# Kernel tuning notes

Hardware: AMD Instinct MI355X
Metric: run time of the kernel (lower is better)

## Reference

```python
import jax, jax.numpy as jnp
import numpy as np

B = 8192
D, T = 40, 100      # input_dim = [D, T]
P, Q = 120, 100     # output_dim = [P, Q]


def setup_inputs() -> dict:
    key = jax.random.key(0)
    ks = jax.random.split(key, 6)
    s = 0.05  # keep pre-softmax logits in a sane range
    return {
        "X": jax.random.normal(ks[0], (B, D, T), dtype=jnp.float32),
        "W1": jax.random.normal(ks[1], (P, D), dtype=jnp.float32) * s,
        "W": jax.random.normal(ks[2], (T, T), dtype=jnp.float32) * s,
        "alpha": jax.random.uniform(ks[3], (1,), dtype=jnp.float32),
        "W2": jax.random.normal(ks[4], (T, Q), dtype=jnp.float32) * s,
        "bias": jax.random.normal(ks[5], (P, Q), dtype=jnp.float32) * s,
    }


def reference(X, W1, W, alpha, W2, bias):
    # X: [B, D, T]
    X1 = jnp.einsum("pd,bdt->bpt", W1, X)          # per-sample W1 @ X[i]
    E = jnp.einsum("bpt,ts->bps", X1, W)            # per-sample X1[i] @ W
    # Faithful to torch: nn.Softmax() with dim=None on a 3D tensor -> dim 0 (batch)
    A = jax.nn.softmax(E, axis=0)                   # [B, P, T]
    tem = alpha * (X1 * A) + (1.0 - alpha) * X1     # alpha-gated attention blend
    Y = jnp.einsum("bpt,tq->bpq", tem, W2) + bias   # [B, P, Q]
    # output_dim[1] == Q == 100 != 1, so the squeeze branch is not taken
    return Y
```

## Files before the change

### kernel.cpp

```cpp
#include <hip/hip_runtime.h>


typedef __attribute__((ext_vector_type(8))) short short8;
typedef __attribute__((ext_vector_type(4))) float floatx4;

constexpr int Bb = 8192;

constexpr int ST1 = 136;
constexpr int ST2 = 72;

constexpr int XB_B   = 48  * ST1 * 2;
constexpr int XWT_B  = 112 * ST2 * 2;
constexpr int WT_B   = 112 * ST1 * 2;
constexpr int W2T_B  = 112 * ST1 * 2;
constexpr int XT_B   = 112 * ST2 * 2;
constexpr int X1A_B  = 128 * ST1 * 2;

constexpr int WS_S_BYTES = 48000;
constexpr int WTG_OFF  = 48000;
constexpr int W1G_OFF  = WTG_OFF + WT_B;
constexpr int W2TG_OFF = W1G_OFF + 128 * ST2 * 2;

constexpr int P1_XB  = 0;
constexpr int P1_XWT = XB_B;
constexpr int P1_WT  = P1_XWT + XWT_B;
constexpr int P1_LDS = P1_WT + WT_B;

constexpr int P2_WB  = X1A_B;
constexpr int P2_LDS = P2_WB + WT_B;

constexpr int NB1 = 16;
constexpr int NB2 = 32;

constexpr int WCHUNKS = WT_B / 16;

__device__ __forceinline__ unsigned short f2bf(float f) {
  union { float f; unsigned u; } v; v.f = f;
  return (unsigned short)((v.u + 0x7FFFu + ((v.u >> 16) & 1u)) >> 16);
}

__device__ __forceinline__ void copy16(void* dst, const void* src, int nbytes,
                                       int tid, int nthr) {
  int4* d = (int4*)dst; const int4* s = (const int4*)src;
  const int n = nbytes >> 4;
  for (int i = tid; i < n; i += nthr) d[i] = s[i];
}

__global__ void tabl_prep(const float* __restrict__ W1, const float* __restrict__ W,
                          const float* __restrict__ W2, char* ws) {
  int i = blockIdx.x * 256 + threadIdx.x;
  if (i < 112 * ST1) {
    int s = i / ST1, t = i % ST1;
    ((unsigned short*)(ws + WTG_OFF))[i] = (s < 100 && t < 100) ? f2bf(W[t * 100 + s]) : 0;
  } else if (i < 112 * ST1 + 128 * ST2) {
    int j = i - 112 * ST1;
    int p = j / ST2, d = j % ST2;
    ((unsigned short*)(ws + W1G_OFF))[j] = (p < 120 && d < 40) ? f2bf(W1[p * 40 + d]) : 0;
  } else if (i < 112 * ST1 + 128 * ST2 + 112 * ST1) {
    int j = i - 112 * ST1 - 128 * ST2;
    int q = j / ST1, t = j % ST1;
    ((unsigned short*)(ws + W2TG_OFF))[j] = (q < 100 && t < 100) ? f2bf(W2[t * 100 + q]) : 0;
  }
}

__global__ __launch_bounds__(256, 2)
void tabl_ph1(const float* __restrict__ X, const char* __restrict__ ws,
              float* __restrict__ S) {
  __shared__ __align__(16) char smem[P1_LDS];
  short* Xb  = (short*)(smem + P1_XB);
  short* XWt = (short*)(smem + P1_XWT);
  short* Wt  = (short*)(smem + P1_WT);

  const int tid = threadIdx.x;
  const int wid = tid >> 6, lane = tid & 63;
  const int quad = lane >> 4, r = lane & 15;
  const floatx4 zed = {0.f, 0.f, 0.f, 0.f};

  short8 w1f[2][2];
#pragma unroll
  for (int h = 0; h < 2; ++h)
#pragma unroll
    for (int ks = 0; ks < 2; ++ks)
      w1f[h][ks] = *(const short8*)(ws + W1G_OFF +
          2 * (((2 * wid + h) * 16 + r) * ST2 + ks * 32 + quad * 8));

  copy16(Wt, ws + WTG_OFF, WT_B, tid, 256);
  for (int i = tid; i < 8 * ST1; i += 256) {
    int dd = 40 + i / ST1, tt = i % ST1; Xb[dd * ST1 + tt] = 0;
  }
  for (int i = tid; i < 40 * 28; i += 256) {
    int dd = i / 28, tt = 100 + i % 28; Xb[dd * ST1 + tt] = 0;
  }
  for (int i = tid; i < 112 * 16; i += 256) {
    int rr = i / 16, cc = 48 + i % 16; XWt[rr * ST2 + cc] = 0;
  }

  const int b0 = blockIdx.x * NB1;
  {
    const float4* x4 = (const float4*)(X + (size_t)b0 * 4000);
#pragma unroll
    for (int k = 0; k < 4; ++k) {
      int idx = tid + k * 256;
      if (idx < 1000) {
        float4 v = x4[idx];
        short4 pk; pk.x = (short)f2bf(v.x); pk.y = (short)f2bf(v.y);
        pk.z = (short)f2bf(v.z); pk.w = (short)f2bf(v.w);
        int e0 = idx * 4, d = e0 / 100, t = e0 - d * 100;
        *(short4*)&Xb[d * ST1 + t] = pk;
      }
    }
  }

  floatx4 sacc[2][7];
#pragma unroll
  for (int h = 0; h < 2; ++h)
#pragma unroll
    for (int n = 0; n < 7; ++n) sacc[h][n] = zed;

  for (int nb = 0; nb < NB1; ++nb) {
    __syncthreads();

    float4 xr[4];
    const bool pf = (nb + 1 < NB1);
    if (pf) {
      const float4* x4n = (const float4*)(X + (size_t)(b0 + nb + 1) * 4000);
#pragma unroll
      for (int k = 0; k < 4; ++k) {
        int idx = tid + k * 256;
        if (idx < 1000) xr[k] = x4n[idx];
      }
    }

    floatx4 xw[2][3];
#pragma unroll
    for (int ns = 0; ns < 2; ++ns)
#pragma unroll
      for (int m = 0; m < 3; ++m) xw[ns][m] = zed;
#pragma unroll
    for (int ks = 0; ks < 4; ++ks) {
      short8 a0 = *(const short8*)&Xb[(0 * 16 + r) * ST1 + ks * 32 + quad * 8];
      short8 a1 = *(const short8*)&Xb[(1 * 16 + r) * ST1 + ks * 32 + quad * 8];
      short8 a2 = *(const short8*)&Xb[(2 * 16 + r) * ST1 + ks * 32 + quad * 8];
#pragma unroll
      for (int ns = 0; ns < 2; ++ns) {
        int ni = wid + ns * 4;
        if (ni < 7) {
          short8 bf = *(const short8*)&Wt[(ni * 16 + r) * ST1 + ks * 32 + quad * 8];
          xw[ns][0] = __builtin_amdgcn_mfma_f32_16x16x32_bf16(a0, bf, xw[ns][0], 0, 0, 0);
          xw[ns][1] = __builtin_amdgcn_mfma_f32_16x16x32_bf16(a1, bf, xw[ns][1], 0, 0, 0);
          xw[ns][2] = __builtin_amdgcn_mfma_f32_16x16x32_bf16(a2, bf, xw[ns][2], 0, 0, 0);
        }
      }
    }
#pragma unroll
    for (int ns = 0; ns < 2; ++ns) {
      int ni = wid + ns * 4;
      if (ni < 7) {
#pragma unroll
        for (int m = 0; m < 3; ++m) {
          short4 pk;
          pk.x = (short)f2bf(xw[ns][m][0]); pk.y = (short)f2bf(xw[ns][m][1]);
          pk.z = (short)f2bf(xw[ns][m][2]); pk.w = (short)f2bf(xw[ns][m][3]);
          *(short4*)&XWt[(ni * 16 + r) * ST2 + m * 16 + quad * 4] = pk;
        }
      }
    }
    __syncthreads();

#pragma unroll
    for (int n = 0; n < 7; ++n) {
      floatx4 e0 = zed, e1 = zed;
#pragma unroll
      for (int ks = 0; ks < 2; ++ks) {
        short8 bf = *(const short8*)&XWt[(n * 16 + r) * ST2 + ks * 32 + quad * 8];
        e0 = __builtin_amdgcn_mfma_f32_16x16x32_bf16(w1f[0][ks], bf, e0, 0, 0, 0);
        e1 = __builtin_amdgcn_mfma_f32_16x16x32_bf16(w1f[1][ks], bf, e1, 0, 0, 0);
      }
#pragma unroll
      for (int c = 0; c < 4; ++c) {
        sacc[0][n][c] += __expf(e0[c]);
        sacc[1][n][c] += __expf(e1[c]);
      }
    }

    if (pf) {
#pragma unroll
      for (int k = 0; k < 4; ++k) {
        int idx = tid + k * 256;
        if (idx < 1000) {
          short4 pk; pk.x = (short)f2bf(xr[k].x); pk.y = (short)f2bf(xr[k].y);
          pk.z = (short)f2bf(xr[k].z); pk.w = (short)f2bf(xr[k].w);
          int e0 = idx * 4, d = e0 / 100, t = e0 - d * 100;
          *(short4*)&Xb[d * ST1 + t] = pk;
        }
      }
    }
  }

#pragma unroll
  for (int h = 0; h < 2; ++h) {
    int mi = 2 * wid + h;
#pragma unroll
    for (int n = 0; n < 7; ++n) {
      int s = n * 16 + r;
#pragma unroll
      for (int c = 0; c < 4; ++c) {
        int p = mi * 16 + quad * 4 + c;
        if (p < 120 && s < 100) atomicAdd(&S[p * 100 + s], sacc[h][n][c]);
      }
    }
  }
}

__global__ __launch_bounds__(512, 2)
void tabl_ph2(const float* __restrict__ X, const char* __restrict__ ws,
              const float* __restrict__ alphap, const float* __restrict__ bias,
              float* __restrict__ Y) {
  __shared__ __align__(16) char smem[P2_LDS];
  short* Xt   = (short*)(smem);
  short* X1A  = (short*)(smem);
  short* Wbuf = (short*)(smem + P2_WB);
  const float* S = (const float*)ws;

  const int tid = threadIdx.x;
  const int wid = tid >> 6, lane = tid & 63;
  const int quad = lane >> 4, r = lane & 15;
  const int mp = wid & 3, nh = wid >> 2;
  const int NJ = nh ? 3 : 4;
  const floatx4 zed = {0.f, 0.f, 0.f, 0.f};
  const int4 iz = {0, 0, 0, 0};

  const int b0 = blockIdx.x * NB2;
  const float alpha = alphap[0];
  const float oma = 1.f - alpha;

  floatx4 sinv[2][4], br[2][4];
#pragma unroll
  for (int h = 0; h < 2; ++h)
#pragma unroll
    for (int j = 0; j < 4; ++j) {
      int n = nh * 4 + j;
      int s = n * 16 + r;
#pragma unroll
      for (int c = 0; c < 4; ++c) {
        int p = (2 * mp + h) * 16 + quad * 4 + c;
        bool ok = (j < NJ) && (p < 120) && (s < 100);
        sinv[h][j][c] = ok ? alpha / S[p * 100 + s] : 0.f;
        br[h][j][c]   = ok ? bias[p * 100 + s] : 0.f;
      }
    }

  short8 w1f[2][2];
#pragma unroll
  for (int h = 0; h < 2; ++h)
#pragma unroll
    for (int ks = 0; ks < 2; ++ks)
      w1f[h][ks] = *(const short8*)(ws + W1G_OFF +
          2 * (((2 * mp + h) * 16 + r) * ST2 + ks * 32 + quad * 8));

  copy16(Wbuf, ws + WTG_OFF, WT_B, tid, 512);
  if (tid < 108) ((int4*)Xt)[900 + tid] = iz;
  for (int z = tid; z < 300; z += 512) {
    int t = z / 3, u = z - 3 * t;
    ((int4*)Xt)[t * 9 + 5 + u] = iz;
  }
  {
    const float4* x4 = (const float4*)(X + (size_t)b0 * 4000);
#pragma unroll
    for (int k = 0; k < 2; ++k) {
      int idx = tid + k * 512;
      if (idx < 1000) {
        float4 v = x4[idx];
        int e0 = idx * 4, d = e0 / 100, t0 = e0 - d * 100;
        Xt[(t0 + 0) * ST2 + d] = (short)f2bf(v.x);
        Xt[(t0 + 1) * ST2 + d] = (short)f2bf(v.y);
        Xt[(t0 + 2) * ST2 + d] = (short)f2bf(v.z);
        Xt[(t0 + 3) * ST2 + d] = (short)f2bf(v.w);
      }
    }
  }

  for (int i = 0; i < NB2; ++i) {
    __syncthreads();

    float4 xr[2];
    const bool pf = (i + 1 < NB2);
    if (pf) {
      const float4* x4n = (const float4*)(X + (size_t)(b0 + i + 1) * 4000);
#pragma unroll
      for (int k = 0; k < 2; ++k) {
        int idx = tid + k * 512;
        if (idx < 1000) xr[k] = x4n[idx];
      }
    }

    floatx4 x1[2][4];
#pragma unroll
    for (int h = 0; h < 2; ++h)
#pragma unroll
      for (int j = 0; j < 4; ++j) x1[h][j] = zed;
#pragma unroll
    for (int j = 0; j < 4; ++j) {
      if (j < NJ) {
        int n = nh * 4 + j;
#pragma unroll
        for (int ks = 0; ks < 2; ++ks) {
          short8 bf = *(const short8*)&Xt[(n * 16 + r) * ST2 + ks * 32 + quad * 8];
          x1[0][j] = __builtin_amdgcn_mfma_f32_16x16x32_bf16(w1f[0][ks], bf, x1[0][j], 0, 0, 0);
          x1[1][j] = __builtin_amdgcn_mfma_f32_16x16x32_bf16(w1f[1][ks], bf, x1[1][j], 0, 0, 0);
        }
      }
    }
    __syncthreads();

    int4 wreg[4];
#pragma unroll
    for (int k = 0; k < 4; ++k) {
      int idx = tid + k * 512;
      if (idx < WCHUNKS) wreg[k] = ((const int4*)(ws + W2TG_OFF))[idx];
    }

    if (tid < 256) {
      int row = tid >> 1, half = tid & 1;
      *(int4*)(smem + row * 272 + 224 + half * 16) = iz;
    }
#pragma unroll
    for (int h = 0; h < 2; ++h)
#pragma unroll
      for (int j = 0; j < 4; ++j) {
        if (j < NJ) {
          int t = (nh * 4 + j) * 16 + r;
          int p0 = (2 * mp + h) * 16 + quad * 4;
#pragma unroll
          for (int c = 0; c < 4; ++c)
            X1A[(p0 + c) * ST1 + t] = (short)f2bf(x1[h][j][c]);
        }
      }
    __syncthreads();

    short8 af[2][4];
#pragma unroll
    for (int h = 0; h < 2; ++h)
#pragma unroll
      for (int ks = 0; ks < 4; ++ks)
        af[h][ks] = *(const short8*)&X1A[((2 * mp + h) * 16 + r) * ST1 + ks * 32 + quad * 8];
#pragma unroll
    for (int j = 0; j < 4; ++j) {
      if (j < NJ) {
        int n = nh * 4 + j;
        floatx4 e0 = zed, e1 = zed;
#pragma unroll
        for (int ks = 0; ks < 4; ++ks) {
          short8 bf = *(const short8*)&Wbuf[(n * 16 + r) * ST1 + ks * 32 + quad * 8];
          e0 = __builtin_amdgcn_mfma_f32_16x16x32_bf16(af[0][ks], bf, e0, 0, 0, 0);
          e1 = __builtin_amdgcn_mfma_f32_16x16x32_bf16(af[1][ks], bf, e1, 0, 0, 0);
        }
#pragma unroll
        for (int c = 0; c < 4; ++c) {
          x1[0][j][c] = x1[0][j][c] * (oma + __expf(e0[c]) * sinv[0][j][c]);
          x1[1][j][c] = x1[1][j][c] * (oma + __expf(e1[c]) * sinv[1][j][c]);
        }
      }
    }
    __syncthreads();

#pragma unroll
    for (int h = 0; h < 2; ++h)
#pragma unroll
      for (int j = 0; j < 4; ++j) {
        if (j < NJ) {
          int t = (nh * 4 + j) * 16 + r;
          int p0 = (2 * mp + h) * 16 + quad * 4;
#pragma unroll
          for (int c = 0; c < 4; ++c)
            X1A[(p0 + c) * ST1 + t] = (short)f2bf(x1[h][j][c]);
        }
      }
#pragma unroll
    for (int k = 0; k < 4; ++k) {
      int idx = tid + k * 512;
      if (idx < WCHUNKS) ((int4*)Wbuf)[idx] = wreg[k];
    }
    __syncthreads();

    if (pf) {
#pragma unroll
      for (int k = 0; k < 4; ++k) {
        int idx = tid + k * 512;
        if (idx < WCHUNKS) wreg[k] = ((const int4*)(ws + WTG_OFF))[idx];
      }
    }

#pragma unroll
    for (int h = 0; h < 2; ++h)
#pragma unroll
      for (int ks = 0; ks < 4; ++ks)
        af[h][ks] = *(const short8*)&X1A[((2 * mp + h) * 16 + r) * ST1 + ks * 32 + quad * 8];
    float* Yb = Y + (size_t)(b0 + i) * 12000;
#pragma unroll
    for (int j = 0; j < 4; ++j) {
      if (j < NJ) {
        int n = nh * 4 + j;
        floatx4 y0 = br[0][j], y1 = br[1][j];
#pragma unroll
        for (int ks = 0; ks < 4; ++ks) {
          short8 bf = *(const short8*)&Wbuf[(n * 16 + r) * ST1 + ks * 32 + quad * 8];
          y0 = __builtin_amdgcn_mfma_f32_16x16x32_bf16(af[0][ks], bf, y0, 0, 0, 0);
          y1 = __builtin_amdgcn_mfma_f32_16x16x32_bf16(af[1][ks], bf, y1, 0, 0, 0);
        }
        int qc = n * 16 + r;
        if (qc < 100) {
          int p0 = (2 * mp) * 16 + quad * 4;
#pragma unroll
          for (int c = 0; c < 4; ++c) Yb[(p0 + c) * 100 + qc] = y0[c];
          int p1 = (2 * mp + 1) * 16 + quad * 4;
#pragma unroll
          for (int c = 0; c < 4; ++c)
            if (p1 + c < 120) Yb[(p1 + c) * 100 + qc] = y1[c];
        }
      }
    }
    __syncthreads();

    if (pf) {
      if (tid < 108) ((int4*)Xt)[900 + tid] = iz;
      for (int z = tid; z < 300; z += 512) {
        int t = z / 3, u = z - 3 * t;
        ((int4*)Xt)[t * 9 + 5 + u] = iz;
      }
#pragma unroll
      for (int k = 0; k < 2; ++k) {
        int idx = tid + k * 512;
        if (idx < 1000) {
          float4 v = xr[k];
          int e0 = idx * 4, d = e0 / 100, t0 = e0 - d * 100;
          Xt[(t0 + 0) * ST2 + d] = (short)f2bf(v.x);
          Xt[(t0 + 1) * ST2 + d] = (short)f2bf(v.y);
          Xt[(t0 + 2) * ST2 + d] = (short)f2bf(v.z);
          Xt[(t0 + 3) * ST2 + d] = (short)f2bf(v.w);
        }
      }
#pragma unroll
      for (int k = 0; k < 4; ++k) {
        int idx = tid + k * 512;
        if (idx < WCHUNKS) ((int4*)Wbuf)[idx] = wreg[k];
      }
    }
  }
}

extern "C" void kernel_launch(void* const* d_in, const int* in_sizes, int n_in,
                              void* d_out, int out_size, void* d_ws, size_t ws_size,
                              hipStream_t stream) {
  const float* X    = (const float*)d_in[0];
  const float* W1   = (const float*)d_in[1];
  const float* W    = (const float*)d_in[2];
  const float* al   = (const float*)d_in[3];
  const float* W2   = (const float*)d_in[4];
  const float* bias = (const float*)d_in[5];
  float* Y = (float*)d_out;
  char* ws = (char*)d_ws;

  hipMemsetAsync(ws, 0, WS_S_BYTES, stream);
  int prep_elems = 112 * ST1 + 128 * ST2 + 112 * ST1;
  tabl_prep<<<(prep_elems + 255) / 256, 256, 0, stream>>>(W1, W, W2, ws);
  tabl_ph1<<<Bb / NB1, 256, 0, stream>>>(X, ws, (float*)ws);
  tabl_ph2<<<Bb / NB2, 512, 0, stream>>>(X, ws, al, bias, Y);
}
```

Measured before the change: 763.1 us.

## Swizzle LDS layouts, keep W fragments in registers, shrink batches per block

Phase 2 now stores the transposed X tile and the X1*A tile in LDS through an XOR swizzle on 16-byte chunks, to cut bank conflicts on the MFMA fragment reads and the scattered bf16 writes. Phase 1 loads its W^T MFMA fragments straight into registers and drops the LDS copy of W, which shrinks LDS use. Samples per block are halved in both phases and the occupancy hints in launch bounds are raised. The trade-off is more register pressure in phase 1, more blocks and more atomics on S, and extra address arithmetic for the swizzle.

```diff
diff --git a/kernel.cpp b/kernel.cpp
--- a/kernel.cpp
+++ b/kernel.cpp
@@ -12,8 +12,6 @@
 constexpr int XB_B   = 48  * ST1 * 2;
 constexpr int XWT_B  = 112 * ST2 * 2;
 constexpr int WT_B   = 112 * ST1 * 2;
-constexpr int W2T_B  = 112 * ST1 * 2;
-constexpr int XT_B   = 112 * ST2 * 2;
 constexpr int X1A_B  = 128 * ST1 * 2;
 
 constexpr int WS_S_BYTES = 48000;
@@ -23,14 +21,13 @@
 
 constexpr int P1_XB  = 0;
 constexpr int P1_XWT = XB_B;
-constexpr int P1_WT  = P1_XWT + XWT_B;
-constexpr int P1_LDS = P1_WT + WT_B;
+constexpr int P1_LDS = P1_XWT + XWT_B;
 
 constexpr int P2_WB  = X1A_B;
 constexpr int P2_LDS = P2_WB + WT_B;
 
-constexpr int NB1 = 16;
-constexpr int NB2 = 32;
+constexpr int NB1 = 8;
+constexpr int NB2 = 16;
 
 constexpr int WCHUNKS = WT_B / 16;
 
@@ -44,6 +41,13 @@
   int4* d = (int4*)dst; const int4* s = (const int4*)src;
   const int n = nbytes >> 4;
   for (int i = tid; i < n; i += nthr) d[i] = s[i];
+}
+
+__device__ __forceinline__ int swz1(int row, int off) {
+  return row * 272 + (off ^ (((row >> 2) & 7) << 4));
+}
+__device__ __forceinline__ int swz2(int row, int off) {
+  return row * 144 + (off ^ (((row >> 2) & 7) << 4));
 }
 
 __global__ void tabl_prep(const float* __restrict__ W1, const float* __restrict__ W,
@@ -63,19 +67,27 @@
   }
 }
 
-__global__ __launch_bounds__(256, 2)
+__global__ __launch_bounds__(256, 3)
 void tabl_ph1(const float* __restrict__ X, const char* __restrict__ ws,
               float* __restrict__ S) {
   __shared__ __align__(16) char smem[P1_LDS];
   short* Xb  = (short*)(smem + P1_XB);
   short* XWt = (short*)(smem + P1_XWT);
-  short* Wt  = (short*)(smem + P1_WT);
 
   const int tid = threadIdx.x;
   const int wid = tid >> 6, lane = tid & 63;
   const int quad = lane >> 4, r = lane & 15;
   const floatx4 zed = {0.f, 0.f, 0.f, 0.f};
 
+  short8 wtf[2][4];
+#pragma unroll
+  for (int ns = 0; ns < 2; ++ns) {
+    int ni = wid + ns * 4; int nc = ni < 7 ? ni : 0;
+#pragma unroll
+    for (int ks = 0; ks < 4; ++ks)
+      wtf[ns][ks] = *(const short8*)(ws + WTG_OFF +
+          2 * ((nc * 16 + r) * ST1 + ks * 32 + quad * 8));
+  }
   short8 w1f[2][2];
 #pragma unroll
   for (int h = 0; h < 2; ++h)
@@ -84,7 +96,6 @@
       w1f[h][ks] = *(const short8*)(ws + W1G_OFF +
           2 * (((2 * wid + h) * 16 + r) * ST2 + ks * 32 + quad * 8));
 
-  copy16(Wt, ws + WTG_OFF, WT_B, tid, 256);
   for (int i = tid; i < 8 * ST1; i += 256) {
     int dd = 40 + i / ST1, tt = i % ST1; Xb[dd * ST1 + tt] = 0;
   }
@@ -143,12 +154,10 @@
       short8 a2 = *(const short8*)&Xb[(2 * 16 + r) * ST1 + ks * 32 + quad * 8];
 #pragma unroll
       for (int ns = 0; ns < 2; ++ns) {
-        int ni = wid + ns * 4;
-        if (ni < 7) {
-          short8 bf = *(const short8*)&Wt[(ni * 16 + r) * ST1 + ks * 32 + quad * 8];
-          xw[ns][0] = __builtin_amdgcn_mfma_f32_16x16x32_bf16(a0, bf, xw[ns][0], 0, 0, 0);
-          xw[ns][1] = __builtin_amdgcn_mfma_f32_16x16x32_bf16(a1, bf, xw[ns][1], 0, 0, 0);
-          xw[ns][2] = __builtin_amdgcn_mfma_f32_16x16x32_bf16(a2, bf, xw[ns][2], 0, 0, 0);
+        if (wid + ns * 4 < 7) {
+          xw[ns][0] = __builtin_amdgcn_mfma_f32_16x16x32_bf16(a0, wtf[ns][ks], xw[ns][0], 0, 0, 0);
+          xw[ns][1] = __builtin_amdgcn_mfma_f32_16x16x32_bf16(a1, wtf[ns][ks], xw[ns][1], 0, 0, 0);
+          xw[ns][2] = __builtin_amdgcn_mfma_f32_16x16x32_bf16(a2, wtf[ns][ks], xw[ns][2], 0, 0, 0);
         }
       }
     }
@@ -212,13 +221,11 @@
   }
 }
 
-__global__ __launch_bounds__(512, 2)
+__global__ __launch_bounds__(512, 4)
 void tabl_ph2(const float* __restrict__ X, const char* __restrict__ ws,
               const float* __restrict__ alphap, const float* __restrict__ bias,
               float* __restrict__ Y) {
   __shared__ __align__(16) char smem[P2_LDS];
-  short* Xt   = (short*)(smem);
-  short* X1A  = (short*)(smem);
   short* Wbuf = (short*)(smem + P2_WB);
   const float* S = (const float*)ws;
 
@@ -259,10 +266,13 @@
           2 * (((2 * mp + h) * 16 + r) * ST2 + ks * 32 + quad * 8));
 
   copy16(Wbuf, ws + WTG_OFF, WT_B, tid, 512);
-  if (tid < 108) ((int4*)Xt)[900 + tid] = iz;
+  if (tid < 96) {
+    int row = 100 + (tid >> 3), off = (tid & 7) << 4;
+    *(int4*)(smem + swz2(row, off)) = iz;
+  }
   for (int z = tid; z < 300; z += 512) {
     int t = z / 3, u = z - 3 * t;
-    ((int4*)Xt)[t * 9 + 5 + u] = iz;
+    *(int4*)(smem + swz2(t, 80 + (u << 4))) = iz;
   }
   {
     const float4* x4 = (const float4*)(X + (size_t)b0 * 4000);
@@ -272,10 +282,10 @@
       if (idx < 1000) {
         float4 v = x4[idx];
         int e0 = idx * 4, d = e0 / 100, t0 = e0 - d * 100;
-        Xt[(t0 + 0) * ST2 + d] = (short)f2bf(v.x);
-        Xt[(t0 + 1) * ST2 + d] = (short)f2bf(v.y);
-        Xt[(t0 + 2) * ST2 + d] = (short)f2bf(v.z);
-        Xt[(t0 + 3) * ST2 + d] = (short)f2bf(v.w);
+        *(short*)(smem + swz2(t0 + 0, 2 * d)) = (short)f2bf(v.x);
+        *(short*)(smem + swz2(t0 + 1, 2 * d)) = (short)f2bf(v.y);
+        *(short*)(smem + swz2(t0 + 2, 2 * d)) = (short)f2bf(v.z);
+        *(short*)(smem + swz2(t0 + 3, 2 * d)) = (short)f2bf(v.w);
       }
     }
   }
@@ -305,7 +315,7 @@
         int n = nh * 4 + j;
 #pragma unroll
         for (int ks = 0; ks < 2; ++ks) {
-          short8 bf = *(const short8*)&Xt[(n * 16 + r) * ST2 + ks * 32 + quad * 8];
+          short8 bf = *(const short8*)(smem + swz2(n * 16 + r, ks * 64 + quad * 16));
           x1[0][j] = __builtin_amdgcn_mfma_f32_16x16x32_bf16(w1f[0][ks], bf, x1[0][j], 0, 0, 0);
           x1[1][j] = __builtin_amdgcn_mfma_f32_16x16x32_bf16(w1f[1][ks], bf, x1[1][j], 0, 0, 0);
         }
@@ -321,8 +331,8 @@
     }
 
     if (tid < 256) {
-      int row = tid >> 1, half = tid & 1;
-      *(int4*)(smem + row * 272 + 224 + half * 16) = iz;
+      int row = tid >> 1, off = 224 + ((tid & 1) << 4);
+      *(int4*)(smem + swz1(row, off)) = iz;
     }
 #pragma unroll
     for (int h = 0; h < 2; ++h)
@@ -333,7 +343,7 @@
           int p0 = (2 * mp + h) * 16 + quad * 4;
 #pragma unroll
           for (int c = 0; c < 4; ++c)
-            X1A[(p0 + c) * ST1 + t] = (short)f2bf(x1[h][j][c]);
+            *(short*)(smem + swz1(p0 + c, 2 * t)) = (short)f2bf(x1[h][j][c]);
         }
       }
     __syncthreads();
@@ -343,7 +353,8 @@
     for (int h = 0; h < 2; ++h)
 #pragma unroll
       for (int ks = 0; ks < 4; ++ks)
-        af[h][ks] = *(const short8*)&X1A[((2 * mp + h) * 16 + r) * ST1 + ks * 32 + quad * 8];
+        af[h][ks] = *(const short8*)(smem +
+            swz1((2 * mp + h) * 16 + r, ks * 64 + quad * 16));
 #pragma unroll
     for (int j = 0; j < 4; ++j) {
       if (j < NJ) {
@@ -373,7 +384,7 @@
           int p0 = (2 * mp + h) * 16 + quad * 4;
 #pragma unroll
           for (int c = 0; c < 4; ++c)
-            X1A[(p0 + c) * ST1 + t] = (short)f2bf(x1[h][j][c]);
+            *(short*)(smem + swz1(p0 + c, 2 * t)) = (short)f2bf(x1[h][j][c]);
         }
       }
 #pragma unroll
@@ -395,7 +406,8 @@
     for (int h = 0; h < 2; ++h)
 #pragma unroll
       for (int ks = 0; ks < 4; ++ks)
-        af[h][ks] = *(const short8*)&X1A[((2 * mp + h) * 16 + r) * ST1 + ks * 32 + quad * 8];
+        af[h][ks] = *(const short8*)(smem +
+            swz1((2 * mp + h) * 16 + r, ks * 64 + quad * 16));
     float* Yb = Y + (size_t)(b0 + i) * 12000;
 #pragma unroll
     for (int j = 0; j < 4; ++j) {
@@ -423,10 +435,13 @@
     __syncthreads();
 
     if (pf) {
-      if (tid < 108) ((int4*)Xt)[900 + tid] = iz;
+      if (tid < 96) {
+        int row = 100 + (tid >> 3), off = (tid & 7) << 4;
+        *(int4*)(smem + swz2(row, off)) = iz;
+      }
       for (int z = tid; z < 300; z += 512) {
         int t = z / 3, u = z - 3 * t;
-        ((int4*)Xt)[t * 9 + 5 + u] = iz;
+        *(int4*)(smem + swz2(t, 80 + (u << 4))) = iz;
       }
 #pragma unroll
       for (int k = 0; k < 2; ++k) {
@@ -434,10 +449,10 @@
         if (idx < 1000) {
           float4 v = xr[k];
           int e0 = idx * 4, d = e0 / 100, t0 = e0 - d * 100;
-          Xt[(t0 + 0) * ST2 + d] = (short)f2bf(v.x);
-          Xt[(t0 + 1) * ST2 + d] = (short)f2bf(v.y);
-          Xt[(t0 + 2) * ST2 + d] = (short)f2bf(v.z);
-          Xt[(t0 + 3) * ST2 + d] = (short)f2bf(v.w);
+          *(short*)(smem + swz2(t0 + 0, 2 * d)) = (short)f2bf(v.x);
+          *(short*)(smem + swz2(t0 + 1, 2 * d)) = (short)f2bf(v.y);
+          *(short*)(smem + swz2(t0 + 2, 2 * d)) = (short)f2bf(v.z);
+          *(short*)(smem + swz2(t0 + 3, 2 * d)) = (short)f2bf(v.w);
         }
       }
 #pragma unroll
```

Result: slower. 1.845 ms (+141.8%).
